# Kernel optimization log

Hardware: AMD Instinct MI355X
Metric: run time of the kernel (lower is better)

Reference implementation:

```python
import jax, jax.numpy as jnp
import numpy as np

E, T, A, H = 64, 128, 32, 4
S, O, QH1, QD, C1 = 256, 128, 128, 64, 128  # state, obs, query hidden, query/key dim, c hidden


def setup_inputs() -> dict:
    key = jax.random.key(0)
    ks = jax.random.split(key, 10)
    w = 0.02
    return {
        "q_values": jax.random.normal(ks[0], (E, T, A), jnp.float32),
        "states": jax.random.normal(ks[1], (E, T, S), jnp.float32),
        "individual_fs": jax.random.normal(ks[2], (E, T, A, O), jnp.float32),
        "Wq1": jax.random.normal(ks[3], (S, QH1), jnp.float32) * w,
        "bq1": jnp.zeros((QH1,), jnp.float32),
        "Wq2": jax.random.normal(ks[4], (QH1, QD), jnp.float32) * w,
        "bq2": jnp.zeros((QD,), jnp.float32),
        "Wk": jax.random.normal(ks[5], (H, O, QD), jnp.float32) * w,
        "bk": jnp.zeros((H, QD), jnp.float32),
        "Wc1": jax.random.normal(ks[6], (S, C1), jnp.float32) * w,
        "bc1": jnp.zeros((C1,), jnp.float32),
        "Wc2": jax.random.normal(ks[7], (C1, 1), jnp.float32) * w,
        "bc2": jnp.zeros((1,), jnp.float32),
    }


def reference(q_values, states, individual_fs, Wq1, bq1, Wq2, bq2, Wk, bk, Wc1, bc1, Wc2, bc2):
    e, t, a = q_values.shape
    s = states.reshape(-1, states.shape[-1])              # (B, S), B = E*T
    f = individual_fs.reshape(e * t, a, -1)               # (B, A, O)
    # query embedding of state: 2-layer MLP with ReLU
    emb_s = jnp.maximum(s @ Wq1 + bq1, 0.0) @ Wq2 + bq2   # (B, QD)
    # all-agents, all-heads key extraction in one batched einsum
    emb_u = jnp.einsum('bao,hok->bahk', f, Wk) + bk       # (B, A, H, QD)
    # query-key dot products per agent/head, then sum over heads
    Lambda_i = jnp.einsum('bk,bahk->bah', emb_s, emb_u).sum(axis=-1)  # (B, A)
    # state-dependent scalar bias
    c_value = jnp.maximum(s @ Wc1 + bc1, 0.0) @ Wc2 + bc2  # (B, 1)
    Q_tot = jnp.sum(Lambda_i * q_values.reshape(-1, a), axis=-1, keepdims=True) + c_value
    return Q_tot.reshape(e, t, 1)
```

## Files before the change

kernel.cpp:

```cpp
#include <hip/hip_runtime.h>


static constexpr int Sd  = 256;
static constexpr int Ad  = 32;
static constexpr int Od  = 128;
static constexpr int QDd = 64;
static constexpr int NB  = 16;
static constexpr int A_BLOCKS = 512;
static constexpr int B_BLOCKS = 1024;

__global__ void qatten_prep(const float* __restrict__ Wk, const float* __restrict__ bk,
                            float* __restrict__ WkT, float* __restrict__ bkSum)
{
    int idx = blockIdx.x * 256 + threadIdx.x;
    int k = idx >> 7;
    int o = idx & 127;
    float s = 0.f;
#pragma unroll
    for (int h = 0; h < 4; ++h) s += Wk[h * (Od * QDd) + o * QDd + k];
    WkT[k * Od + o] = s;
    if (idx < QDd) {
        float t = 0.f;
#pragma unroll
        for (int h = 0; h < 4; ++h) t += bk[h * QDd + idx];
        bkSum[idx] = t;
    }
}

__global__ __launch_bounds__(256, 4) void qatten_main(
    const float* __restrict__ qv, const float* __restrict__ st, const float* __restrict__ fs,
    const float* __restrict__ Wq1, const float* __restrict__ bq1,
    const float* __restrict__ Wq2, const float* __restrict__ bq2,
    const float* __restrict__ Wc1, const float* __restrict__ bc1,
    const float* __restrict__ Wc2, const float* __restrict__ bc2,
    const float* __restrict__ WkT, const float* __restrict__ bkSum,
    float* __restrict__ v_out, float* __restrict__ bias_out, float* __restrict__ g_out)
{
    __shared__ float s_lds[NB][Sd];
    __shared__ float h_lds[NB][260];
    __shared__ float emb_lds[NB][68];

    const int tid = threadIdx.x;

    if (blockIdx.x < A_BLOCKS) {
        const int b0 = blockIdx.x * NB;

        {
            const float4* sp = (const float4*)(st + (size_t)b0 * Sd);
            float4* sl = (float4*)&s_lds[0][0];
            sl[tid]       = sp[tid];
            sl[tid + 256] = sp[tid + 256];
            sl[tid + 512] = sp[tid + 512];
            sl[tid + 768] = sp[tid + 768];
        }
        __syncthreads();

        {
            const int wg = tid & 63;
            const int rg = (tid >> 6) << 2;
            const float* __restrict__ Wb = (wg < 32) ? (Wq1 + 4 * wg)
                                                     : (Wc1 + 4 * (wg - 32));
            const float4 bb4 = (wg < 32) ? *(const float4*)&bq1[4 * wg]
                                         : *(const float4*)&bc1[4 * (wg - 32)];
            float acc[4][4];
#pragma unroll
            for (int r = 0; r < 4; ++r)
#pragma unroll
                for (int c = 0; c < 4; ++c) acc[r][c] = 0.f;

            for (int k = 0; k < Sd; k += 4) {
                float w[4][4], sv[4][4];
#pragma unroll
                for (int kk = 0; kk < 4; ++kk) {
                    const float4 t = *(const float4*)&Wb[(size_t)(k + kk) * 128];
                    w[kk][0] = t.x; w[kk][1] = t.y; w[kk][2] = t.z; w[kk][3] = t.w;
                }
#pragma unroll
                for (int r = 0; r < 4; ++r) {
                    const float4 t = *(const float4*)&s_lds[rg + r][k];
                    sv[r][0] = t.x; sv[r][1] = t.y; sv[r][2] = t.z; sv[r][3] = t.w;
                }
#pragma unroll
                for (int r = 0; r < 4; ++r)
#pragma unroll
                    for (int kk = 0; kk < 4; ++kk)
#pragma unroll
                        for (int c = 0; c < 4; ++c)
                            acc[r][c] = fmaf(sv[r][kk], w[kk][c], acc[r][c]);
            }
#pragma unroll
            for (int r = 0; r < 4; ++r) {
                float4 o;
                o.x = fmaxf(acc[r][0] + bb4.x, 0.f);
                o.y = fmaxf(acc[r][1] + bb4.y, 0.f);
                o.z = fmaxf(acc[r][2] + bb4.z, 0.f);
                o.w = fmaxf(acc[r][3] + bb4.w, 0.f);
                *(float4*)&h_lds[rg + r][4 * wg] = o;
            }
        }
        __syncthreads();

        {
            const int cg = tid & 15;
            const int row = tid >> 4;
            float acc[4] = {0.f, 0.f, 0.f, 0.f};
            for (int k = 0; k < 128; k += 4) {
                float w[4][4];
#pragma unroll
                for (int kk = 0; kk < 4; ++kk) {
                    const float4 t = *(const float4*)&Wq2[(size_t)(k + kk) * 64 + 4 * cg];
                    w[kk][0] = t.x; w[kk][1] = t.y; w[kk][2] = t.z; w[kk][3] = t.w;
                }
                const float4 h4 = *(const float4*)&h_lds[row][k];
                float hv[4] = {h4.x, h4.y, h4.z, h4.w};
#pragma unroll
                for (int kk = 0; kk < 4; ++kk)
#pragma unroll
                    for (int c = 0; c < 4; ++c)
                        acc[c] = fmaf(hv[kk], w[kk][c], acc[c]);
            }
            const float4 b4 = *(const float4*)&bq2[4 * cg];
            float4 o;
            o.x = acc[0] + b4.x; o.y = acc[1] + b4.y;
            o.z = acc[2] + b4.z; o.w = acc[3] + b4.w;
            *(float4*)&emb_lds[row][4 * cg] = o;
        }
        __syncthreads();

        {
            const int cg = tid & 31;
            const int rp = (tid >> 5) << 1;
            float acc[2][4];
#pragma unroll
            for (int r = 0; r < 2; ++r)
#pragma unroll
                for (int c = 0; c < 4; ++c) acc[r][c] = 0.f;
            for (int k = 0; k < QDd; k += 4) {
                float w[4][4], ev[2][4];
#pragma unroll
                for (int kk = 0; kk < 4; ++kk) {
                    const float4 t = *(const float4*)&WkT[(size_t)(k + kk) * 128 + 4 * cg];
                    w[kk][0] = t.x; w[kk][1] = t.y; w[kk][2] = t.z; w[kk][3] = t.w;
                }
#pragma unroll
                for (int r = 0; r < 2; ++r) {
                    const float4 t = *(const float4*)&emb_lds[rp + r][k];
                    ev[r][0] = t.x; ev[r][1] = t.y; ev[r][2] = t.z; ev[r][3] = t.w;
                }
#pragma unroll
                for (int r = 0; r < 2; ++r)
#pragma unroll
                    for (int kk = 0; kk < 4; ++kk)
#pragma unroll
                        for (int c = 0; c < 4; ++c)
                            acc[r][c] = fmaf(ev[r][kk], w[kk][c], acc[r][c]);
            }
#pragma unroll
            for (int r = 0; r < 2; ++r) {
                float4 o;
                o.x = acc[r][0]; o.y = acc[r][1]; o.z = acc[r][2]; o.w = acc[r][3];
                *(float4*)&v_out[(size_t)(b0 + rp + r) * Od + 4 * cg] = o;
            }
        }

        {
            const int b = tid >> 4;
            const int i = tid & 15;
            float pb = 0.f, pc = 0.f;
#pragma unroll
            for (int k = i; k < QDd; k += 16)  pb = fmaf(emb_lds[b][k], bkSum[k], pb);
#pragma unroll
            for (int j = i; j < 128; j += 16)  pc = fmaf(h_lds[b][128 + j], Wc2[j], pc);
            float pq = qv[(size_t)(b0 + b) * Ad + i] + qv[(size_t)(b0 + b) * Ad + i + 16];
#pragma unroll
            for (int d = 8; d >= 1; d >>= 1) {
                pb += __shfl_down(pb, d, 16);
                pc += __shfl_down(pc, d, 16);
                pq += __shfl_down(pq, d, 16);
            }
            if (i == 0) bias_out[b0 + b] = (pc + bc2[0]) + pb * pq;
        }
    } else {
        const int w = tid >> 6;
        const int l = tid & 63;
        const int r0 = ((int)blockIdx.x - A_BLOCKS) * 8 + w * 2;
        const float4* __restrict__ f0 = (const float4*)fs + (size_t)r0 * (Ad * Od / 4);
        const float4* __restrict__ f1 = f0 + (Ad * Od / 4);
        const float q0 = qv[(size_t)r0 * Ad + (l & 31)];
        const float q1 = qv[(size_t)(r0 + 1) * Ad + (l & 31)];
        float4 a0 = {0.f, 0.f, 0.f, 0.f}, a1 = {0.f, 0.f, 0.f, 0.f};
#pragma unroll
        for (int i = 0; i < 16; ++i) {
            const float4 x0 = f0[i * 64 + l];
            const float4 x1 = f1[i * 64 + l];
            const float qa0 = __shfl(q0, 2 * i + (l >> 5), 64);
            const float qa1 = __shfl(q1, 2 * i + (l >> 5), 64);
            a0.x = fmaf(qa0, x0.x, a0.x);
            a0.y = fmaf(qa0, x0.y, a0.y);
            a0.z = fmaf(qa0, x0.z, a0.z);
            a0.w = fmaf(qa0, x0.w, a0.w);
            a1.x = fmaf(qa1, x1.x, a1.x);
            a1.y = fmaf(qa1, x1.y, a1.y);
            a1.z = fmaf(qa1, x1.z, a1.z);
            a1.w = fmaf(qa1, x1.w, a1.w);
        }
        a0.x += __shfl_xor(a0.x, 32, 64);
        a0.y += __shfl_xor(a0.y, 32, 64);
        a0.z += __shfl_xor(a0.z, 32, 64);
        a0.w += __shfl_xor(a0.w, 32, 64);
        a1.x += __shfl_xor(a1.x, 32, 64);
        a1.y += __shfl_xor(a1.y, 32, 64);
        a1.z += __shfl_xor(a1.z, 32, 64);
        a1.w += __shfl_xor(a1.w, 32, 64);
        if (l < 32) {
            *(float4*)(g_out + (size_t)r0 * Od + l * 4) = a0;
            *(float4*)(g_out + (size_t)(r0 + 1) * Od + l * 4) = a1;
        }
    }
}

__global__ __launch_bounds__(256, 8) void qatten_final(
    const float* __restrict__ g, const float* __restrict__ v,
    const float* __restrict__ bias, float* __restrict__ out)
{
    const int tid = threadIdx.x;
    const int b = blockIdx.x * 8 + (tid >> 5);
    const int i = tid & 31;
    const float4 gv = *(const float4*)(g + (size_t)b * Od + i * 4);
    const float4 vv = *(const float4*)(v + (size_t)b * Od + i * 4);
    float d = gv.x * vv.x;
    d = fmaf(gv.y, vv.y, d);
    d = fmaf(gv.z, vv.z, d);
    d = fmaf(gv.w, vv.w, d);
#pragma unroll
    for (int k = 16; k >= 1; k >>= 1) d += __shfl_down(d, k, 32);
    if (i == 0) out[b] = d + bias[b];
}

extern "C" void kernel_launch(void* const* d_in, const int* in_sizes, int n_in,
                              void* d_out, int out_size, void* d_ws, size_t ws_size,
                              hipStream_t stream) {
    const float* qv  = (const float*)d_in[0];
    const float* st  = (const float*)d_in[1];
    const float* fs  = (const float*)d_in[2];
    const float* Wq1 = (const float*)d_in[3];
    const float* bq1 = (const float*)d_in[4];
    const float* Wq2 = (const float*)d_in[5];
    const float* bq2 = (const float*)d_in[6];
    const float* Wk  = (const float*)d_in[7];
    const float* bk  = (const float*)d_in[8];
    const float* Wc1 = (const float*)d_in[9];
    const float* bc1 = (const float*)d_in[10];
    const float* Wc2 = (const float*)d_in[11];
    const float* bc2 = (const float*)d_in[12];
    float* out = (float*)d_out;

    float* WkT   = (float*)d_ws;
    float* bkSum = WkT + QDd * Od;
    float* bias  = bkSum + QDd;
    float* vbuf  = bias + 8192;
    float* gbuf  = vbuf + 8192 * Od;

    qatten_prep<<<32, 256, 0, stream>>>(Wk, bk, WkT, bkSum);
    qatten_main<<<A_BLOCKS + B_BLOCKS, 256, 0, stream>>>(
        qv, st, fs, Wq1, bq1, Wq2, bq2, Wc1, bc1, Wc2, bc2,
        WkT, bkSum, vbuf, bias, gbuf);
    qatten_final<<<1024, 256, 0, stream>>>(gbuf, vbuf, bias, out);
}
```

Baseline: 242.8 us.

## Split g reduction into own kernel and fuse final dot into MLP kernel

```diff
diff --git a/kernel.cpp b/kernel.cpp
--- a/kernel.cpp
+++ b/kernel.cpp
@@ -6,8 +6,8 @@
 static constexpr int Od  = 128;
 static constexpr int QDd = 64;
 static constexpr int NB  = 16;
-static constexpr int A_BLOCKS = 512;
-static constexpr int B_BLOCKS = 1024;
+static constexpr int MLP_BLOCKS = 512;
+static constexpr int G_BLOCKS   = 2048;
 
 __global__ void qatten_prep(const float* __restrict__ Wk, const float* __restrict__ bk,
                             float* __restrict__ WkT, float* __restrict__ bkSum)
@@ -27,214 +27,169 @@
     }
 }
 
-__global__ __launch_bounds__(256, 4) void qatten_main(
-    const float* __restrict__ qv, const float* __restrict__ st, const float* __restrict__ fs,
+__global__ __launch_bounds__(256, 8) void qatten_g(
+    const float* __restrict__ qv, const float* __restrict__ fs,
+    float* __restrict__ g_out)
+{
+    const int w = threadIdx.x >> 6;
+    const int l = threadIdx.x & 63;
+    const int b = blockIdx.x * 4 + w;
+    const float4* __restrict__ fb = (const float4*)fs + (size_t)b * (Ad * Od / 4);
+    const float qreg = qv[(size_t)b * Ad + (l & 31)];
+    float4 acc = {0.f, 0.f, 0.f, 0.f};
+#pragma unroll
+    for (int i = 0; i < 16; ++i) {
+        const float4 f4 = fb[i * 64 + l];
+        const float  qa = __shfl(qreg, 2 * i + (l >> 5), 64);
+        acc.x = fmaf(qa, f4.x, acc.x);
+        acc.y = fmaf(qa, f4.y, acc.y);
+        acc.z = fmaf(qa, f4.z, acc.z);
+        acc.w = fmaf(qa, f4.w, acc.w);
+    }
+    acc.x += __shfl_xor(acc.x, 32, 64);
+    acc.y += __shfl_xor(acc.y, 32, 64);
+    acc.z += __shfl_xor(acc.z, 32, 64);
+    acc.w += __shfl_xor(acc.w, 32, 64);
+    if (l < 32)
+        *(float4*)(g_out + (size_t)b * Od + l * 4) = acc;
+}
+
+__global__ __launch_bounds__(512, 4) void qatten_mlp(
+    const float* __restrict__ qv, const float* __restrict__ st,
     const float* __restrict__ Wq1, const float* __restrict__ bq1,
     const float* __restrict__ Wq2, const float* __restrict__ bq2,
     const float* __restrict__ Wc1, const float* __restrict__ bc1,
     const float* __restrict__ Wc2, const float* __restrict__ bc2,
     const float* __restrict__ WkT, const float* __restrict__ bkSum,
-    float* __restrict__ v_out, float* __restrict__ bias_out, float* __restrict__ g_out)
+    const float* __restrict__ g_in, float* __restrict__ out)
 {
     __shared__ float s_lds[NB][Sd];
     __shared__ float h_lds[NB][260];
     __shared__ float emb_lds[NB][68];
 
     const int tid = threadIdx.x;
-
-    if (blockIdx.x < A_BLOCKS) {
-        const int b0 = blockIdx.x * NB;
-
-        {
-            const float4* sp = (const float4*)(st + (size_t)b0 * Sd);
-            float4* sl = (float4*)&s_lds[0][0];
-            sl[tid]       = sp[tid];
-            sl[tid + 256] = sp[tid + 256];
-            sl[tid + 512] = sp[tid + 512];
-            sl[tid + 768] = sp[tid + 768];
-        }
-        __syncthreads();
-
-        {
-            const int wg = tid & 63;
-            const int rg = (tid >> 6) << 2;
-            const float* __restrict__ Wb = (wg < 32) ? (Wq1 + 4 * wg)
-                                                     : (Wc1 + 4 * (wg - 32));
-            const float4 bb4 = (wg < 32) ? *(const float4*)&bq1[4 * wg]
-                                         : *(const float4*)&bc1[4 * (wg - 32)];
-            float acc[4][4];
-#pragma unroll
-            for (int r = 0; r < 4; ++r)
-#pragma unroll
-                for (int c = 0; c < 4; ++c) acc[r][c] = 0.f;
-
-            for (int k = 0; k < Sd; k += 4) {
-                float w[4][4], sv[4][4];
-#pragma unroll
-                for (int kk = 0; kk < 4; ++kk) {
-                    const float4 t = *(const float4*)&Wb[(size_t)(k + kk) * 128];
-                    w[kk][0] = t.x; w[kk][1] = t.y; w[kk][2] = t.z; w[kk][3] = t.w;
-                }
-#pragma unroll
-                for (int r = 0; r < 4; ++r) {
-                    const float4 t = *(const float4*)&s_lds[rg + r][k];
-                    sv[r][0] = t.x; sv[r][1] = t.y; sv[r][2] = t.z; sv[r][3] = t.w;
-                }
-#pragma unroll
-                for (int r = 0; r < 4; ++r)
-#pragma unroll
-                    for (int kk = 0; kk < 4; ++kk)
-#pragma unroll
-                        for (int c = 0; c < 4; ++c)
-                            acc[r][c] = fmaf(sv[r][kk], w[kk][c], acc[r][c]);
-            }
-#pragma unroll
-            for (int r = 0; r < 4; ++r) {
-                float4 o;
-                o.x = fmaxf(acc[r][0] + bb4.x, 0.f);
-                o.y = fmaxf(acc[r][1] + bb4.y, 0.f);
-                o.z = fmaxf(acc[r][2] + bb4.z, 0.f);
-                o.w = fmaxf(acc[r][3] + bb4.w, 0.f);
-                *(float4*)&h_lds[rg + r][4 * wg] = o;
-            }
-        }
-        __syncthreads();
-
-        {
-            const int cg = tid & 15;
-            const int row = tid >> 4;
-            float acc[4] = {0.f, 0.f, 0.f, 0.f};
-            for (int k = 0; k < 128; k += 4) {
-                float w[4][4];
-#pragma unroll
-                for (int kk = 0; kk < 4; ++kk) {
-                    const float4 t = *(const float4*)&Wq2[(size_t)(k + kk) * 64 + 4 * cg];
-                    w[kk][0] = t.x; w[kk][1] = t.y; w[kk][2] = t.z; w[kk][3] = t.w;
-                }
-                const float4 h4 = *(const float4*)&h_lds[row][k];
-                float hv[4] = {h4.x, h4.y, h4.z, h4.w};
+    const int b0 = blockIdx.x * NB;
+
+    {
+        const float4* sp = (const float4*)(st + (size_t)b0 * Sd);
+        float4* sl = (float4*)&s_lds[0][0];
+        sl[tid]       = sp[tid];
+        sl[tid + 512] = sp[tid + 512];
+    }
+    __syncthreads();
+
+    {
+        const int wg = tid & 63;
+        const int rg = (tid >> 6) << 1;
+        const float* __restrict__ Wb = (wg < 32) ? (Wq1 + 4 * wg)
+                                                 : (Wc1 + 4 * (wg - 32));
+        const float4 bb4 = (wg < 32) ? *(const float4*)&bq1[4 * wg]
+                                     : *(const float4*)&bc1[4 * (wg - 32)];
+        float acc[2][4];
+#pragma unroll
+        for (int r = 0; r < 2; ++r)
+#pragma unroll
+            for (int c = 0; c < 4; ++c) acc[r][c] = 0.f;
+
+        for (int k = 0; k < Sd; k += 4) {
+            float w[4][4], sv[2][4];
+#pragma unroll
+            for (int kk = 0; kk < 4; ++kk) {
+                const float4 t = *(const float4*)&Wb[(size_t)(k + kk) * 128];
+                w[kk][0] = t.x; w[kk][1] = t.y; w[kk][2] = t.z; w[kk][3] = t.w;
+            }
+#pragma unroll
+            for (int r = 0; r < 2; ++r) {
+                const float4 t = *(const float4*)&s_lds[rg + r][k];
+                sv[r][0] = t.x; sv[r][1] = t.y; sv[r][2] = t.z; sv[r][3] = t.w;
+            }
+#pragma unroll
+            for (int r = 0; r < 2; ++r)
 #pragma unroll
                 for (int kk = 0; kk < 4; ++kk)
 #pragma unroll
                     for (int c = 0; c < 4; ++c)
-                        acc[c] = fmaf(hv[kk], w[kk][c], acc[c]);
-            }
-            const float4 b4 = *(const float4*)&bq2[4 * cg];
+                        acc[r][c] = fmaf(sv[r][kk], w[kk][c], acc[r][c]);
+        }
+#pragma unroll
+        for (int r = 0; r < 2; ++r) {
             float4 o;
-            o.x = acc[0] + b4.x; o.y = acc[1] + b4.y;
-            o.z = acc[2] + b4.z; o.w = acc[3] + b4.w;
-            *(float4*)&emb_lds[row][4 * cg] = o;
-        }
-        __syncthreads();
-
-        {
-            const int cg = tid & 31;
-            const int rp = (tid >> 5) << 1;
-            float acc[2][4];
-#pragma unroll
-            for (int r = 0; r < 2; ++r)
-#pragma unroll
-                for (int c = 0; c < 4; ++c) acc[r][c] = 0.f;
-            for (int k = 0; k < QDd; k += 4) {
-                float w[4][4], ev[2][4];
-#pragma unroll
-                for (int kk = 0; kk < 4; ++kk) {
-                    const float4 t = *(const float4*)&WkT[(size_t)(k + kk) * 128 + 4 * cg];
-                    w[kk][0] = t.x; w[kk][1] = t.y; w[kk][2] = t.z; w[kk][3] = t.w;
-                }
-#pragma unroll
-                for (int r = 0; r < 2; ++r) {
-                    const float4 t = *(const float4*)&emb_lds[rp + r][k];
-                    ev[r][0] = t.x; ev[r][1] = t.y; ev[r][2] = t.z; ev[r][3] = t.w;
-                }
-#pragma unroll
-                for (int r = 0; r < 2; ++r)
-#pragma unroll
-                    for (int kk = 0; kk < 4; ++kk)
-#pragma unroll
-                        for (int c = 0; c < 4; ++c)
-                            acc[r][c] = fmaf(ev[r][kk], w[kk][c], acc[r][c]);
-            }
-#pragma unroll
-            for (int r = 0; r < 2; ++r) {
-                float4 o;
-                o.x = acc[r][0]; o.y = acc[r][1]; o.z = acc[r][2]; o.w = acc[r][3];
-                *(float4*)&v_out[(size_t)(b0 + rp + r) * Od + 4 * cg] = o;
-            }
-        }
-
-        {
-            const int b = tid >> 4;
-            const int i = tid & 15;
-            float pb = 0.f, pc = 0.f;
-#pragma unroll
-            for (int k = i; k < QDd; k += 16)  pb = fmaf(emb_lds[b][k], bkSum[k], pb);
-#pragma unroll
-            for (int j = i; j < 128; j += 16)  pc = fmaf(h_lds[b][128 + j], Wc2[j], pc);
-            float pq = qv[(size_t)(b0 + b) * Ad + i] + qv[(size_t)(b0 + b) * Ad + i + 16];
-#pragma unroll
-            for (int d = 8; d >= 1; d >>= 1) {
-                pb += __shfl_down(pb, d, 16);
-                pc += __shfl_down(pc, d, 16);
-                pq += __shfl_down(pq, d, 16);
-            }
-            if (i == 0) bias_out[b0 + b] = (pc + bc2[0]) + pb * pq;
-        }
-    } else {
-        const int w = tid >> 6;
-        const int l = tid & 63;
-        const int r0 = ((int)blockIdx.x - A_BLOCKS) * 8 + w * 2;
-        const float4* __restrict__ f0 = (const float4*)fs + (size_t)r0 * (Ad * Od / 4);
-        const float4* __restrict__ f1 = f0 + (Ad * Od / 4);
-        const float q0 = qv[(size_t)r0 * Ad + (l & 31)];
-        const float q1 = qv[(size_t)(r0 + 1) * Ad + (l & 31)];
-        float4 a0 = {0.f, 0.f, 0.f, 0.f}, a1 = {0.f, 0.f, 0.f, 0.f};
-#pragma unroll
-        for (int i = 0; i < 16; ++i) {
-            const float4 x0 = f0[i * 64 + l];
-            const float4 x1 = f1[i * 64 + l];
-            const float qa0 = __shfl(q0, 2 * i + (l >> 5), 64);
-            const float qa1 = __shfl(q1, 2 * i + (l >> 5), 64);
-            a0.x = fmaf(qa0, x0.x, a0.x);
-            a0.y = fmaf(qa0, x0.y, a0.y);
-            a0.z = fmaf(qa0, x0.z, a0.z);
-            a0.w = fmaf(qa0, x0.w, a0.w);
-            a1.x = fmaf(qa1, x1.x, a1.x);
-            a1.y = fmaf(qa1, x1.y, a1.y);
-            a1.z = fmaf(qa1, x1.z, a1.z);
-            a1.w = fmaf(qa1, x1.w, a1.w);
-        }
-        a0.x += __shfl_xor(a0.x, 32, 64);
-        a0.y += __shfl_xor(a0.y, 32, 64);
-        a0.z += __shfl_xor(a0.z, 32, 64);
-        a0.w += __shfl_xor(a0.w, 32, 64);
-        a1.x += __shfl_xor(a1.x, 32, 64);
-        a1.y += __shfl_xor(a1.y, 32, 64);
-        a1.z += __shfl_xor(a1.z, 32, 64);
-        a1.w += __shfl_xor(a1.w, 32, 64);
-        if (l < 32) {
-            *(float4*)(g_out + (size_t)r0 * Od + l * 4) = a0;
-            *(float4*)(g_out + (size_t)(r0 + 1) * Od + l * 4) = a1;
-        }
-    }
-}
-
-__global__ __launch_bounds__(256, 8) void qatten_final(
-    const float* __restrict__ g, const float* __restrict__ v,
-    const float* __restrict__ bias, float* __restrict__ out)
-{
-    const int tid = threadIdx.x;
-    const int b = blockIdx.x * 8 + (tid >> 5);
-    const int i = tid & 31;
-    const float4 gv = *(const float4*)(g + (size_t)b * Od + i * 4);
-    const float4 vv = *(const float4*)(v + (size_t)b * Od + i * 4);
-    float d = gv.x * vv.x;
-    d = fmaf(gv.y, vv.y, d);
-    d = fmaf(gv.z, vv.z, d);
-    d = fmaf(gv.w, vv.w, d);
-#pragma unroll
-    for (int k = 16; k >= 1; k >>= 1) d += __shfl_down(d, k, 32);
-    if (i == 0) out[b] = d + bias[b];
+            o.x = fmaxf(acc[r][0] + bb4.x, 0.f);
+            o.y = fmaxf(acc[r][1] + bb4.y, 0.f);
+            o.z = fmaxf(acc[r][2] + bb4.z, 0.f);
+            o.w = fmaxf(acc[r][3] + bb4.w, 0.f);
+            *(float4*)&h_lds[rg + r][4 * wg] = o;
+        }
+    }
+    __syncthreads();
+
+    {
+        const int c2  = tid & 31;
+        const int row = tid >> 5;
+        float a0 = 0.f, a1 = 0.f;
+        for (int k = 0; k < 128; k += 4) {
+            float2 w[4];
+#pragma unroll
+            for (int kk = 0; kk < 4; ++kk)
+                w[kk] = *(const float2*)&Wq2[(size_t)(k + kk) * 64 + 2 * c2];
+            const float4 h4 = *(const float4*)&h_lds[row][k];
+            a0 = fmaf(h4.x, w[0].x, a0);  a1 = fmaf(h4.x, w[0].y, a1);
+            a0 = fmaf(h4.y, w[1].x, a0);  a1 = fmaf(h4.y, w[1].y, a1);
+            a0 = fmaf(h4.z, w[2].x, a0);  a1 = fmaf(h4.z, w[2].y, a1);
+            a0 = fmaf(h4.w, w[3].x, a0);  a1 = fmaf(h4.w, w[3].y, a1);
+        }
+        const float2 b2 = *(const float2*)&bq2[2 * c2];
+        float2 o; o.x = a0 + b2.x; o.y = a1 + b2.y;
+        *(float2*)&emb_lds[row][2 * c2] = o;
+    }
+    __syncthreads();
+
+    {
+        const int cg  = tid & 31;
+        const int row = tid >> 5;
+        const int b   = b0 + row;
+
+        float acc[4] = {0.f, 0.f, 0.f, 0.f};
+        for (int k = 0; k < QDd; k += 4) {
+            float w[4][4];
+#pragma unroll
+            for (int kk = 0; kk < 4; ++kk) {
+                const float4 t = *(const float4*)&WkT[(size_t)(k + kk) * 128 + 4 * cg];
+                w[kk][0] = t.x; w[kk][1] = t.y; w[kk][2] = t.z; w[kk][3] = t.w;
+            }
+            const float4 e4 = *(const float4*)&emb_lds[row][k];
+#pragma unroll
+            for (int c = 0; c < 4; ++c) {
+                float a = acc[c];
+                a = fmaf(e4.x, w[0][c], a);
+                a = fmaf(e4.y, w[1][c], a);
+                a = fmaf(e4.z, w[2][c], a);
+                a = fmaf(e4.w, w[3][c], a);
+                acc[c] = a;
+            }
+        }
+        const float4 g4 = *(const float4*)&g_in[(size_t)b * Od + 4 * cg];
+        float d = acc[0] * g4.x;
+        d = fmaf(acc[1], g4.y, d);
+        d = fmaf(acc[2], g4.z, d);
+        d = fmaf(acc[3], g4.w, d);
+        float pb = fmaf(emb_lds[row][cg],      bkSum[cg],      0.f);
+        pb       = fmaf(emb_lds[row][cg + 32], bkSum[cg + 32], pb);
+        float pc = 0.f;
+#pragma unroll
+        for (int j = 0; j < 4; ++j)
+            pc = fmaf(h_lds[row][128 + cg + 32 * j], Wc2[cg + 32 * j], pc);
+        float pq = qv[(size_t)b * Ad + cg];
+#pragma unroll
+        for (int dd = 16; dd >= 1; dd >>= 1) {
+            d  += __shfl_down(d,  dd, 32);
+            pb += __shfl_down(pb, dd, 32);
+            pc += __shfl_down(pc, dd, 32);
+            pq += __shfl_down(pq, dd, 32);
+        }
+        if (cg == 0)
+            out[b] = d + (pc + bc2[0]) + pb * pq;
+    }
 }
 
 extern "C" void kernel_launch(void* const* d_in, const int* in_sizes, int n_in,
@@ -257,13 +212,11 @@
 
     float* WkT   = (float*)d_ws;
     float* bkSum = WkT + QDd * Od;
-    float* bias  = bkSum + QDd;
-    float* vbuf  = bias + 8192;
-    float* gbuf  = vbuf + 8192 * Od;
+    float* gbuf  = bkSum + QDd;
 
     qatten_prep<<<32, 256, 0, stream>>>(Wk, bk, WkT, bkSum);
-    qatten_main<<<A_BLOCKS + B_BLOCKS, 256, 0, stream>>>(
-        qv, st, fs, Wq1, bq1, Wq2, bq2, Wc1, bc1, Wc2, bc2,
-        WkT, bkSum, vbuf, bias, gbuf);
-    qatten_final<<<1024, 256, 0, stream>>>(gbuf, vbuf, bias, out);
-}
+    qatten_g<<<G_BLOCKS, 256, 0, stream>>>(qv, fs, gbuf);
+    qatten_mlp<<<MLP_BLOCKS, 512, 0, stream>>>(qv, st, Wq1, bq1, Wq2, bq2,
+                                               Wc1, bc1, Wc2, bc2,
+                                               WkT, bkSum, gbuf, out);
+}
```

New measurement: 282.0 us. 1.16x slower.

## Interleave compute and streaming blocks and software-prefetch weight loads in GEMV loops

Applied to the files above, without the earlier changes.

```diff
diff --git a/kernel.cpp b/kernel.cpp
--- a/kernel.cpp
+++ b/kernel.cpp
@@ -41,9 +41,10 @@
     __shared__ float emb_lds[NB][68];
 
     const int tid = threadIdx.x;
-
-    if (blockIdx.x < A_BLOCKS) {
-        const int b0 = blockIdx.x * NB;
+    const int bid = blockIdx.x;
+
+    if (bid % 3 == 0) {
+        const int b0 = (bid / 3) * NB;
 
         {
             const float4* sp = (const float4*)(st + (size_t)b0 * Sd);
@@ -68,25 +69,46 @@
 #pragma unroll
                 for (int c = 0; c < 4; ++c) acc[r][c] = 0.f;
 
-            for (int k = 0; k < Sd; k += 4) {
-                float w[4][4], sv[4][4];
-#pragma unroll
-                for (int kk = 0; kk < 4; ++kk) {
-                    const float4 t = *(const float4*)&Wb[(size_t)(k + kk) * 128];
-                    w[kk][0] = t.x; w[kk][1] = t.y; w[kk][2] = t.z; w[kk][3] = t.w;
+            float4 wc0 = *(const float4*)&Wb[0];
+            float4 wc1 = *(const float4*)&Wb[128];
+            float4 wc2 = *(const float4*)&Wb[256];
+            float4 wc3 = *(const float4*)&Wb[384];
+
+            for (int k = 0; k < Sd - 4; k += 4) {
+                const float* Wn = Wb + (size_t)(k + 4) * 128;
+                const float4 wn0 = *(const float4*)&Wn[0];
+                const float4 wn1 = *(const float4*)&Wn[128];
+                const float4 wn2 = *(const float4*)&Wn[256];
+                const float4 wn3 = *(const float4*)&Wn[384];
+#pragma unroll
+                for (int r = 0; r < 4; ++r) {
+                    const float4 s4 = *(const float4*)&s_lds[rg + r][k];
+                    float a0 = acc[r][0], a1 = acc[r][1], a2 = acc[r][2], a3 = acc[r][3];
+                    a0 = fmaf(s4.x, wc0.x, a0); a1 = fmaf(s4.x, wc0.y, a1);
+                    a2 = fmaf(s4.x, wc0.z, a2); a3 = fmaf(s4.x, wc0.w, a3);
+                    a0 = fmaf(s4.y, wc1.x, a0); a1 = fmaf(s4.y, wc1.y, a1);
+                    a2 = fmaf(s4.y, wc1.z, a2); a3 = fmaf(s4.y, wc1.w, a3);
+                    a0 = fmaf(s4.z, wc2.x, a0); a1 = fmaf(s4.z, wc2.y, a1);
+                    a2 = fmaf(s4.z, wc2.z, a2); a3 = fmaf(s4.z, wc2.w, a3);
+                    a0 = fmaf(s4.w, wc3.x, a0); a1 = fmaf(s4.w, wc3.y, a1);
+                    a2 = fmaf(s4.w, wc3.z, a2); a3 = fmaf(s4.w, wc3.w, a3);
+                    acc[r][0] = a0; acc[r][1] = a1; acc[r][2] = a2; acc[r][3] = a3;
                 }
-#pragma unroll
-                for (int r = 0; r < 4; ++r) {
-                    const float4 t = *(const float4*)&s_lds[rg + r][k];
-                    sv[r][0] = t.x; sv[r][1] = t.y; sv[r][2] = t.z; sv[r][3] = t.w;
-                }
-#pragma unroll
-                for (int r = 0; r < 4; ++r)
-#pragma unroll
-                    for (int kk = 0; kk < 4; ++kk)
-#pragma unroll
-                        for (int c = 0; c < 4; ++c)
-                            acc[r][c] = fmaf(sv[r][kk], w[kk][c], acc[r][c]);
+                wc0 = wn0; wc1 = wn1; wc2 = wn2; wc3 = wn3;
+            }
+#pragma unroll
+            for (int r = 0; r < 4; ++r) {
+                const float4 s4 = *(const float4*)&s_lds[rg + r][Sd - 4];
+                float a0 = acc[r][0], a1 = acc[r][1], a2 = acc[r][2], a3 = acc[r][3];
+                a0 = fmaf(s4.x, wc0.x, a0); a1 = fmaf(s4.x, wc0.y, a1);
+                a2 = fmaf(s4.x, wc0.z, a2); a3 = fmaf(s4.x, wc0.w, a3);
+                a0 = fmaf(s4.y, wc1.x, a0); a1 = fmaf(s4.y, wc1.y, a1);
+                a2 = fmaf(s4.y, wc1.z, a2); a3 = fmaf(s4.y, wc1.w, a3);
+                a0 = fmaf(s4.z, wc2.x, a0); a1 = fmaf(s4.z, wc2.y, a1);
+                a2 = fmaf(s4.z, wc2.z, a2); a3 = fmaf(s4.z, wc2.w, a3);
+                a0 = fmaf(s4.w, wc3.x, a0); a1 = fmaf(s4.w, wc3.y, a1);
+                a2 = fmaf(s4.w, wc3.z, a2); a3 = fmaf(s4.w, wc3.w, a3);
+                acc[r][0] = a0; acc[r][1] = a1; acc[r][2] = a2; acc[r][3] = a3;
             }
 #pragma unroll
             for (int r = 0; r < 4; ++r) {
@@ -103,26 +125,44 @@
         {
             const int cg = tid & 15;
             const int row = tid >> 4;
-            float acc[4] = {0.f, 0.f, 0.f, 0.f};
-            for (int k = 0; k < 128; k += 4) {
-                float w[4][4];
-#pragma unroll
-                for (int kk = 0; kk < 4; ++kk) {
-                    const float4 t = *(const float4*)&Wq2[(size_t)(k + kk) * 64 + 4 * cg];
-                    w[kk][0] = t.x; w[kk][1] = t.y; w[kk][2] = t.z; w[kk][3] = t.w;
-                }
+            const float* __restrict__ Wb = Wq2 + 4 * cg;
+            float acc0 = 0.f, acc1 = 0.f, acc2 = 0.f, acc3 = 0.f;
+            float4 wc0 = *(const float4*)&Wb[0];
+            float4 wc1 = *(const float4*)&Wb[64];
+            float4 wc2 = *(const float4*)&Wb[128];
+            float4 wc3 = *(const float4*)&Wb[192];
+            for (int k = 0; k < 124; k += 4) {
+                const float* Wn = Wb + (size_t)(k + 4) * 64;
+                const float4 wn0 = *(const float4*)&Wn[0];
+                const float4 wn1 = *(const float4*)&Wn[64];
+                const float4 wn2 = *(const float4*)&Wn[128];
+                const float4 wn3 = *(const float4*)&Wn[192];
                 const float4 h4 = *(const float4*)&h_lds[row][k];
-                float hv[4] = {h4.x, h4.y, h4.z, h4.w};
-#pragma unroll
-                for (int kk = 0; kk < 4; ++kk)
-#pragma unroll
-                    for (int c = 0; c < 4; ++c)
-                        acc[c] = fmaf(hv[kk], w[kk][c], acc[c]);
+                acc0 = fmaf(h4.x, wc0.x, acc0); acc1 = fmaf(h4.x, wc0.y, acc1);
+                acc2 = fmaf(h4.x, wc0.z, acc2); acc3 = fmaf(h4.x, wc0.w, acc3);
+                acc0 = fmaf(h4.y, wc1.x, acc0); acc1 = fmaf(h4.y, wc1.y, acc1);
+                acc2 = fmaf(h4.y, wc1.z, acc2); acc3 = fmaf(h4.y, wc1.w, acc3);
+                acc0 = fmaf(h4.z, wc2.x, acc0); acc1 = fmaf(h4.z, wc2.y, acc1);
+                acc2 = fmaf(h4.z, wc2.z, acc2); acc3 = fmaf(h4.z, wc2.w, acc3);
+                acc0 = fmaf(h4.w, wc3.x, acc0); acc1 = fmaf(h4.w, wc3.y, acc1);
+                acc2 = fmaf(h4.w, wc3.z, acc2); acc3 = fmaf(h4.w, wc3.w, acc3);
+                wc0 = wn0; wc1 = wn1; wc2 = wn2; wc3 = wn3;
+            }
+            {
+                const float4 h4 = *(const float4*)&h_lds[row][124];
+                acc0 = fmaf(h4.x, wc0.x, acc0); acc1 = fmaf(h4.x, wc0.y, acc1);
+                acc2 = fmaf(h4.x, wc0.z, acc2); acc3 = fmaf(h4.x, wc0.w, acc3);
+                acc0 = fmaf(h4.y, wc1.x, acc0); acc1 = fmaf(h4.y, wc1.y, acc1);
+                acc2 = fmaf(h4.y, wc1.z, acc2); acc3 = fmaf(h4.y, wc1.w, acc3);
+                acc0 = fmaf(h4.z, wc2.x, acc0); acc1 = fmaf(h4.z, wc2.y, acc1);
+                acc2 = fmaf(h4.z, wc2.z, acc2); acc3 = fmaf(h4.z, wc2.w, acc3);
+                acc0 = fmaf(h4.w, wc3.x, acc0); acc1 = fmaf(h4.w, wc3.y, acc1);
+                acc2 = fmaf(h4.w, wc3.z, acc2); acc3 = fmaf(h4.w, wc3.w, acc3);
             }
             const float4 b4 = *(const float4*)&bq2[4 * cg];
             float4 o;
-            o.x = acc[0] + b4.x; o.y = acc[1] + b4.y;
-            o.z = acc[2] + b4.z; o.w = acc[3] + b4.w;
+            o.x = acc0 + b4.x; o.y = acc1 + b4.y;
+            o.z = acc2 + b4.z; o.w = acc3 + b4.w;
             *(float4*)&emb_lds[row][4 * cg] = o;
         }
         __syncthreads();
@@ -130,35 +170,51 @@
         {
             const int cg = tid & 31;
             const int rp = (tid >> 5) << 1;
+            const float* __restrict__ Wb = WkT + 4 * cg;
             float acc[2][4];
 #pragma unroll
             for (int r = 0; r < 2; ++r)
 #pragma unroll
                 for (int c = 0; c < 4; ++c) acc[r][c] = 0.f;
-            for (int k = 0; k < QDd; k += 4) {
-                float w[4][4], ev[2][4];
-#pragma unroll
-                for (int kk = 0; kk < 4; ++kk) {
-                    const float4 t = *(const float4*)&WkT[(size_t)(k + kk) * 128 + 4 * cg];
-                    w[kk][0] = t.x; w[kk][1] = t.y; w[kk][2] = t.z; w[kk][3] = t.w;
+            float4 wc0 = *(const float4*)&Wb[0];
+            float4 wc1 = *(const float4*)&Wb[128];
+            float4 wc2 = *(const float4*)&Wb[256];
+            float4 wc3 = *(const float4*)&Wb[384];
+            for (int k = 0; k < QDd - 4; k += 4) {
+                const float* Wn = Wb + (size_t)(k + 4) * 128;
+                const float4 wn0 = *(const float4*)&Wn[0];
+                const float4 wn1 = *(const float4*)&Wn[128];
+                const float4 wn2 = *(const float4*)&Wn[256];
+                const float4 wn3 = *(const float4*)&Wn[384];
+#pragma unroll
+                for (int r = 0; r < 2; ++r) {
+                    const float4 e4 = *(const float4*)&emb_lds[rp + r][k];
+                    float a0 = acc[r][0], a1 = acc[r][1], a2 = acc[r][2], a3 = acc[r][3];
+                    a0 = fmaf(e4.x, wc0.x, a0); a1 = fmaf(e4.x, wc0.y, a1);
+                    a2 = fmaf(e4.x, wc0.z, a2); a3 = fmaf(e4.x, wc0.w, a3);
+                    a0 = fmaf(e4.y, wc1.x, a0); a1 = fmaf(e4.y, wc1.y, a1);
+                    a2 = fmaf(e4.y, wc1.z, a2); a3 = fmaf(e4.y, wc1.w, a3);
+                    a0 = fmaf(e4.z, wc2.x, a0); a1 = fmaf(e4.z, wc2.y, a1);
+                    a2 = fmaf(e4.z, wc2.z, a2); a3 = fmaf(e4.z, wc2.w, a3);
+                    a0 = fmaf(e4.w, wc3.x, a0); a1 = fmaf(e4.w, wc3.y, a1);
+                    a2 = fmaf(e4.w, wc3.z, a2); a3 = fmaf(e4.w, wc3.w, a3);
+                    acc[r][0] = a0; acc[r][1] = a1; acc[r][2] = a2; acc[r][3] = a3;
                 }
-#pragma unroll
-                for (int r = 0; r < 2; ++r) {
-                    const float4 t = *(const float4*)&emb_lds[rp + r][k];
-                    ev[r][0] = t.x; ev[r][1] = t.y; ev[r][2] = t.z; ev[r][3] = t.w;
-                }
-#pragma unroll
-                for (int r = 0; r < 2; ++r)
-#pragma unroll
-                    for (int kk = 0; kk < 4; ++kk)
-#pragma unroll
-                        for (int c = 0; c < 4; ++c)
-                            acc[r][c] = fmaf(ev[r][kk], w[kk][c], acc[r][c]);
+                wc0 = wn0; wc1 = wn1; wc2 = wn2; wc3 = wn3;
             }
 #pragma unroll
             for (int r = 0; r < 2; ++r) {
-                float4 o;
-                o.x = acc[r][0]; o.y = acc[r][1]; o.z = acc[r][2]; o.w = acc[r][3];
+                const float4 e4 = *(const float4*)&emb_lds[rp + r][QDd - 4];
+                float a0 = acc[r][0], a1 = acc[r][1], a2 = acc[r][2], a3 = acc[r][3];
+                a0 = fmaf(e4.x, wc0.x, a0); a1 = fmaf(e4.x, wc0.y, a1);
+                a2 = fmaf(e4.x, wc0.z, a2); a3 = fmaf(e4.x, wc0.w, a3);
+                a0 = fmaf(e4.y, wc1.x, a0); a1 = fmaf(e4.y, wc1.y, a1);
+                a2 = fmaf(e4.y, wc1.z, a2); a3 = fmaf(e4.y, wc1.w, a3);
+                a0 = fmaf(e4.z, wc2.x, a0); a1 = fmaf(e4.z, wc2.y, a1);
+                a2 = fmaf(e4.z, wc2.z, a2); a3 = fmaf(e4.z, wc2.w, a3);
+                a0 = fmaf(e4.w, wc3.x, a0); a1 = fmaf(e4.w, wc3.y, a1);
+                a2 = fmaf(e4.w, wc3.z, a2); a3 = fmaf(e4.w, wc3.w, a3);
+                float4 o; o.x = a0; o.y = a1; o.z = a2; o.w = a3;
                 *(float4*)&v_out[(size_t)(b0 + rp + r) * Od + 4 * cg] = o;
             }
         }
@@ -181,9 +237,10 @@
             if (i == 0) bias_out[b0 + b] = (pc + bc2[0]) + pb * pq;
         }
     } else {
+        const int bidx = bid - (bid / 3) - 1;
         const int w = tid >> 6;
         const int l = tid & 63;
-        const int r0 = ((int)blockIdx.x - A_BLOCKS) * 8 + w * 2;
+        const int r0 = bidx * 8 + w * 2;
         const float4* __restrict__ f0 = (const float4*)fs + (size_t)r0 * (Ad * Od / 4);
         const float4* __restrict__ f1 = f0 + (Ad * Od / 4);
         const float q0 = qv[(size_t)r0 * Ad + (l & 31)];
```

Result: slower. 268.3 us (+10.5%).

## Halve rows per MLP block, alias LDS buffers, interleave MLP and stream blocks

Applied to the files above, without the earlier changes.

```diff
diff --git a/kernel.cpp b/kernel.cpp
--- a/kernel.cpp
+++ b/kernel.cpp
@@ -5,8 +5,8 @@
 static constexpr int Ad  = 32;
 static constexpr int Od  = 128;
 static constexpr int QDd = 64;
-static constexpr int NB  = 16;
-static constexpr int A_BLOCKS = 512;
+static constexpr int NB  = 8;
+static constexpr int A_BLOCKS = 1024;
 static constexpr int B_BLOCKS = 1024;
 
 __global__ void qatten_prep(const float* __restrict__ Wk, const float* __restrict__ bk,
@@ -27,7 +27,12 @@
     }
 }
 
-__global__ __launch_bounds__(256, 4) void qatten_main(
+union SEmb {
+    float s[NB][Sd];
+    float emb[NB][68];
+};
+
+__global__ __launch_bounds__(256, 8) void qatten_main(
     const float* __restrict__ qv, const float* __restrict__ st, const float* __restrict__ fs,
     const float* __restrict__ Wq1, const float* __restrict__ bq1,
     const float* __restrict__ Wq2, const float* __restrict__ bq2,
@@ -36,60 +41,60 @@
     const float* __restrict__ WkT, const float* __restrict__ bkSum,
     float* __restrict__ v_out, float* __restrict__ bias_out, float* __restrict__ g_out)
 {
-    __shared__ float s_lds[NB][Sd];
+    __shared__ SEmb u;
     __shared__ float h_lds[NB][260];
-    __shared__ float emb_lds[NB][68];
 
     const int tid = threadIdx.x;
-
-    if (blockIdx.x < A_BLOCKS) {
-        const int b0 = blockIdx.x * NB;
+    const int bid = blockIdx.x;
+
+    if ((bid & 1) == 0) {
+        const int b0 = (bid >> 1) * NB;
 
         {
             const float4* sp = (const float4*)(st + (size_t)b0 * Sd);
-            float4* sl = (float4*)&s_lds[0][0];
+            float4* sl = (float4*)&u.s[0][0];
             sl[tid]       = sp[tid];
             sl[tid + 256] = sp[tid + 256];
-            sl[tid + 512] = sp[tid + 512];
-            sl[tid + 768] = sp[tid + 768];
         }
         __syncthreads();
 
         {
             const int wg = tid & 63;
-            const int rg = (tid >> 6) << 2;
+            const int rg = (tid >> 6) << 1;
             const float* __restrict__ Wb = (wg < 32) ? (Wq1 + 4 * wg)
                                                      : (Wc1 + 4 * (wg - 32));
             const float4 bb4 = (wg < 32) ? *(const float4*)&bq1[4 * wg]
                                          : *(const float4*)&bc1[4 * (wg - 32)];
-            float acc[4][4];
-#pragma unroll
-            for (int r = 0; r < 4; ++r)
+            float acc[2][4];
+#pragma unroll
+            for (int r = 0; r < 2; ++r)
 #pragma unroll
                 for (int c = 0; c < 4; ++c) acc[r][c] = 0.f;
 
             for (int k = 0; k < Sd; k += 4) {
-                float w[4][4], sv[4][4];
+                float w[4][4];
 #pragma unroll
                 for (int kk = 0; kk < 4; ++kk) {
                     const float4 t = *(const float4*)&Wb[(size_t)(k + kk) * 128];
                     w[kk][0] = t.x; w[kk][1] = t.y; w[kk][2] = t.z; w[kk][3] = t.w;
                 }
 #pragma unroll
-                for (int r = 0; r < 4; ++r) {
-                    const float4 t = *(const float4*)&s_lds[rg + r][k];
-                    sv[r][0] = t.x; sv[r][1] = t.y; sv[r][2] = t.z; sv[r][3] = t.w;
-                }
-#pragma unroll
-                for (int r = 0; r < 4; ++r)
-#pragma unroll
-                    for (int kk = 0; kk < 4; ++kk)
-#pragma unroll
-                        for (int c = 0; c < 4; ++c)
-                            acc[r][c] = fmaf(sv[r][kk], w[kk][c], acc[r][c]);
-            }
-#pragma unroll
-            for (int r = 0; r < 4; ++r) {
+                for (int r = 0; r < 2; ++r) {
+                    const float4 s4 = *(const float4*)&u.s[rg + r][k];
+                    float a0 = acc[r][0], a1 = acc[r][1], a2 = acc[r][2], a3 = acc[r][3];
+                    a0 = fmaf(s4.x, w[0][0], a0); a1 = fmaf(s4.x, w[0][1], a1);
+                    a2 = fmaf(s4.x, w[0][2], a2); a3 = fmaf(s4.x, w[0][3], a3);
+                    a0 = fmaf(s4.y, w[1][0], a0); a1 = fmaf(s4.y, w[1][1], a1);
+                    a2 = fmaf(s4.y, w[1][2], a2); a3 = fmaf(s4.y, w[1][3], a3);
+                    a0 = fmaf(s4.z, w[2][0], a0); a1 = fmaf(s4.z, w[2][1], a1);
+                    a2 = fmaf(s4.z, w[2][2], a2); a3 = fmaf(s4.z, w[2][3], a3);
+                    a0 = fmaf(s4.w, w[3][0], a0); a1 = fmaf(s4.w, w[3][1], a1);
+                    a2 = fmaf(s4.w, w[3][2], a2); a3 = fmaf(s4.w, w[3][3], a3);
+                    acc[r][0] = a0; acc[r][1] = a1; acc[r][2] = a2; acc[r][3] = a3;
+                }
+            }
+#pragma unroll
+            for (int r = 0; r < 2; ++r) {
                 float4 o;
                 o.x = fmaxf(acc[r][0] + bb4.x, 0.f);
                 o.y = fmaxf(acc[r][1] + bb4.y, 0.f);
@@ -101,89 +106,74 @@
         __syncthreads();
 
         {
-            const int cg = tid & 15;
-            const int row = tid >> 4;
+            const int c2  = tid & 31;
+            const int row = tid >> 5;
+            float a0 = 0.f, a1 = 0.f;
+            for (int k = 0; k < 128; k += 4) {
+                float2 w[4];
+#pragma unroll
+                for (int kk = 0; kk < 4; ++kk)
+                    w[kk] = *(const float2*)&Wq2[(size_t)(k + kk) * 64 + 2 * c2];
+                const float4 h4 = *(const float4*)&h_lds[row][k];
+                a0 = fmaf(h4.x, w[0].x, a0);  a1 = fmaf(h4.x, w[0].y, a1);
+                a0 = fmaf(h4.y, w[1].x, a0);  a1 = fmaf(h4.y, w[1].y, a1);
+                a0 = fmaf(h4.z, w[2].x, a0);  a1 = fmaf(h4.z, w[2].y, a1);
+                a0 = fmaf(h4.w, w[3].x, a0);  a1 = fmaf(h4.w, w[3].y, a1);
+            }
+            const float2 b2 = *(const float2*)&bq2[2 * c2];
+            float2 o; o.x = a0 + b2.x; o.y = a1 + b2.y;
+            *(float2*)&u.emb[row][2 * c2] = o;
+        }
+        __syncthreads();
+
+        {
+            const int cg  = tid & 31;
+            const int row = tid >> 5;
             float acc[4] = {0.f, 0.f, 0.f, 0.f};
-            for (int k = 0; k < 128; k += 4) {
+            for (int k = 0; k < QDd; k += 4) {
                 float w[4][4];
-#pragma unroll
-                for (int kk = 0; kk < 4; ++kk) {
-                    const float4 t = *(const float4*)&Wq2[(size_t)(k + kk) * 64 + 4 * cg];
-                    w[kk][0] = t.x; w[kk][1] = t.y; w[kk][2] = t.z; w[kk][3] = t.w;
-                }
-                const float4 h4 = *(const float4*)&h_lds[row][k];
-                float hv[4] = {h4.x, h4.y, h4.z, h4.w};
-#pragma unroll
-                for (int kk = 0; kk < 4; ++kk)
-#pragma unroll
-                    for (int c = 0; c < 4; ++c)
-                        acc[c] = fmaf(hv[kk], w[kk][c], acc[c]);
-            }
-            const float4 b4 = *(const float4*)&bq2[4 * cg];
-            float4 o;
-            o.x = acc[0] + b4.x; o.y = acc[1] + b4.y;
-            o.z = acc[2] + b4.z; o.w = acc[3] + b4.w;
-            *(float4*)&emb_lds[row][4 * cg] = o;
-        }
-        __syncthreads();
-
-        {
-            const int cg = tid & 31;
-            const int rp = (tid >> 5) << 1;
-            float acc[2][4];
-#pragma unroll
-            for (int r = 0; r < 2; ++r)
-#pragma unroll
-                for (int c = 0; c < 4; ++c) acc[r][c] = 0.f;
-            for (int k = 0; k < QDd; k += 4) {
-                float w[4][4], ev[2][4];
 #pragma unroll
                 for (int kk = 0; kk < 4; ++kk) {
                     const float4 t = *(const float4*)&WkT[(size_t)(k + kk) * 128 + 4 * cg];
                     w[kk][0] = t.x; w[kk][1] = t.y; w[kk][2] = t.z; w[kk][3] = t.w;
                 }
-#pragma unroll
-                for (int r = 0; r < 2; ++r) {
-                    const float4 t = *(const float4*)&emb_lds[rp + r][k];
-                    ev[r][0] = t.x; ev[r][1] = t.y; ev[r][2] = t.z; ev[r][3] = t.w;
-                }
-#pragma unroll
-                for (int r = 0; r < 2; ++r)
-#pragma unroll
-                    for (int kk = 0; kk < 4; ++kk)
-#pragma unroll
-                        for (int c = 0; c < 4; ++c)
-                            acc[r][c] = fmaf(ev[r][kk], w[kk][c], acc[r][c]);
-            }
-#pragma unroll
-            for (int r = 0; r < 2; ++r) {
-                float4 o;
-                o.x = acc[r][0]; o.y = acc[r][1]; o.z = acc[r][2]; o.w = acc[r][3];
-                *(float4*)&v_out[(size_t)(b0 + rp + r) * Od + 4 * cg] = o;
-            }
-        }
-
-        {
-            const int b = tid >> 4;
-            const int i = tid & 15;
+                const float4 e4 = *(const float4*)&u.emb[row][k];
+#pragma unroll
+                for (int c = 0; c < 4; ++c) {
+                    float a = acc[c];
+                    a = fmaf(e4.x, w[0][c], a);
+                    a = fmaf(e4.y, w[1][c], a);
+                    a = fmaf(e4.z, w[2][c], a);
+                    a = fmaf(e4.w, w[3][c], a);
+                    acc[c] = a;
+                }
+            }
+            float4 o; o.x = acc[0]; o.y = acc[1]; o.z = acc[2]; o.w = acc[3];
+            *(float4*)&v_out[(size_t)(b0 + row) * Od + 4 * cg] = o;
+        }
+
+        {
+            const int b = tid >> 5;
+            const int i = tid & 31;
             float pb = 0.f, pc = 0.f;
 #pragma unroll
-            for (int k = i; k < QDd; k += 16)  pb = fmaf(emb_lds[b][k], bkSum[k], pb);
-#pragma unroll
-            for (int j = i; j < 128; j += 16)  pc = fmaf(h_lds[b][128 + j], Wc2[j], pc);
-            float pq = qv[(size_t)(b0 + b) * Ad + i] + qv[(size_t)(b0 + b) * Ad + i + 16];
-#pragma unroll
-            for (int d = 8; d >= 1; d >>= 1) {
-                pb += __shfl_down(pb, d, 16);
-                pc += __shfl_down(pc, d, 16);
-                pq += __shfl_down(pq, d, 16);
+            for (int k = i; k < QDd; k += 32)  pb = fmaf(u.emb[b][k], bkSum[k], pb);
+#pragma unroll
+            for (int j = i; j < 128; j += 32)  pc = fmaf(h_lds[b][128 + j], Wc2[j], pc);
+            float pq = qv[(size_t)(b0 + b) * Ad + i];
+#pragma unroll
+            for (int d = 16; d >= 1; d >>= 1) {
+                pb += __shfl_down(pb, d, 32);
+                pc += __shfl_down(pc, d, 32);
+                pq += __shfl_down(pq, d, 32);
             }
             if (i == 0) bias_out[b0 + b] = (pc + bc2[0]) + pb * pq;
         }
     } else {
+        const int bidx = bid >> 1;
         const int w = tid >> 6;
         const int l = tid & 63;
-        const int r0 = ((int)blockIdx.x - A_BLOCKS) * 8 + w * 2;
+        const int r0 = bidx * 8 + w * 2;
         const float4* __restrict__ f0 = (const float4*)fs + (size_t)r0 * (Ad * Od / 4);
         const float4* __restrict__ f1 = f0 + (Ad * Od / 4);
         const float q0 = qv[(size_t)r0 * Ad + (l & 31)];
```

Result: slower. 316.3 us (+30.2%).
